# Optimization experiments

Hardware: AMD Instinct MI355X
Metric: run time of the kernel (lower is better)

The kernel has to match this reference:

```python
import jax, jax.numpy as jnp
import numpy as np
from jax import lax

INV_SQRT2 = np.float32(1.0 / np.sqrt(2.0))

def conv2d(x, w, b=None, stride=1, pad=0):
    y = lax.conv_general_dilated(x, w, (stride, stride), [(pad, pad), (pad, pad)],
                                 dimension_numbers=('NCHW', 'OIHW', 'NCHW'))
    return y if b is None else y + b[None, :, None, None]

def haar_dwt2_zero(x):
    # pytorch_wavelets DWTForward(J=1, wave='haar', mode='zero') for odd H,W:
    # pad one zero at the end of each spatial dim, then pairwise Haar analysis.
    x = jnp.pad(x, ((0, 0), (0, 0), (0, 1), (0, 1)))
    xe, xo = x[..., 0::2], x[..., 1::2]
    lo_w, hi_w = (xe + xo) * INV_SQRT2, (xe - xo) * INV_SQRT2
    def rows(t):
        te, to = t[:, :, 0::2, :], t[:, :, 1::2, :]
        return (te + to) * INV_SQRT2, (te - to) * INV_SQRT2
    ll, lh = rows(lo_w)
    hl, hh = rows(hi_w)
    return ll, lh, hl, hh  # cA, cH, cV, cD

def pixel_shuffle2(x):
    B, C, H, W = x.shape
    co = C // 4
    return x.reshape(B, co, 2, 2, H, W).transpose(0, 1, 4, 2, 5, 3).reshape(B, co, H * 2, W * 2)

def gaussian_kernel5(sigma=0.5):
    r = np.arange(5, dtype=np.float64) - 2.0
    k = np.exp(-(r ** 2) / (2.0 * sigma * sigma))
    return jnp.asarray((k / k.sum()).astype(np.float32))

_GK = gaussian_kernel5(0.5)

def gaussian_blur5(x4d):
    # cv2.GaussianBlur ksize=(5,5) sigma=0.5, default BORDER_REFLECT_101 -> 'reflect' pad
    p = jnp.pad(x4d, ((0, 0), (0, 0), (2, 2), (2, 2)), mode='reflect')
    p = conv2d(p, _GK.reshape(1, 1, 5, 1))
    return conv2d(p, _GK.reshape(1, 1, 1, 5))

def channel_attention(x, w1, w2):
    avg = jnp.mean(x, axis=(2, 3), keepdims=True)
    mx = jnp.max(x, axis=(2, 3), keepdims=True)
    mlp = lambda v: conv2d(jax.nn.relu(conv2d(v, w1)), w2)
    return jax.nn.sigmoid(mlp(avg) + mlp(mx)) * x

def _forward(x, w_x1, b_x1, w_x2, b_x2, w_x3, b_x3, w_hi, b_hi, w_lo, b_lo,
             ca1_w1, ca1_w2, ca2_w1, ca2_w2, w_cat, b_cat, w_c9a, b_c9a, w_c9b, b_c9b):
    f1 = jax.nn.relu(conv2d(x, w_x1, b_x1))            # (1,16,H,W)
    f2 = jax.nn.relu(conv2d(f1, w_x2, b_x2))           # (1,8,H,W)
    tmp12 = jax.nn.relu(conv2d(f2, w_x3, b_x3))        # (1,1,H,W)
    cA, cH, cV, cD = haar_dwt2_zero(tmp12)             # each (1,1,(H+1)/2,(W+1)/2)
    hf = pixel_shuffle2(jax.nn.relu(conv2d(jnp.concatenate([cH, cV, cD], 1), w_hi, b_hi, pad=1)))
    lf = pixel_shuffle2(jax.nn.relu(conv2d(cA, w_lo, b_lo, pad=1)))  # (1,1,H+5,W+5)
    # original detaches hf (cpu->numpy->cv2->cuda): gradients do not flow through it
    hf = gaussian_blur5(lax.stop_gradient(hf))
    hf = channel_attention(hf, ca1_w1, ca1_w2)
    lf = channel_attention(lf, ca2_w1, ca2_w2)
    alpha = 1.0
    cat = jax.nn.relu(conv2d(jnp.concatenate([alpha * hf, (1.0 - alpha) * lf], 1), w_cat, b_cat))
    f12 = tmp12 + cat                                   # (1,1,H,W)
    h = jax.nn.relu(conv2d(f12, w_c9a, b_c9a, pad=1))   # (1,32,H,W)
    return jax.nn.relu(conv2d(h, w_c9b, b_c9b, pad=1))  # (1,64,H,W)

def setup_inputs() -> dict:
    key = jax.random.key(0)
    ks = jax.random.split(key, 24)
    f32 = jnp.float32
    n = lambda k, s, sc=0.05: jax.random.normal(k, s, f32) * sc
    H = W = 511
    return {
        'x': jax.random.normal(ks[0], (1, 204, H, W), f32),
        'w_x1': n(ks[1], (16, 204, 1, 1)), 'b_x1': n(ks[2], (16,)),
        'w_x2': n(ks[3], (8, 16, 1, 1)),   'b_x2': n(ks[4], (8,)),
        'w_x3': n(ks[5], (1, 8, 1, 1)),    'b_x3': n(ks[6], (1,)),
        'w_hi': n(ks[7], (4, 3, 1, 1)),    'b_hi': n(ks[8], (4,)),
        'w_lo': n(ks[9], (4, 1, 1, 1)),    'b_lo': n(ks[10], (4,)),
        'ca1_w1': n(ks[11], (1, 1, 1, 1), 0.5), 'ca1_w2': n(ks[12], (1, 1, 1, 1), 0.5),
        'ca2_w1': n(ks[13], (1, 1, 1, 1), 0.5), 'ca2_w2': n(ks[14], (1, 1, 1, 1), 0.5),
        'w_cat': n(ks[15], (1, 2, 6, 6)),  'b_cat': n(ks[16], (1,)),
        'w_c9a': n(ks[17], (32, 1, 3, 3)), 'b_c9a': n(ks[18], (32,)),
        'w_c9b': n(ks[19], (64, 32, 3, 3)), 'b_c9b': n(ks[20], (64,)),
    }

def reference(x, w_x1, b_x1, w_x2, b_x2, w_x3, b_x3, w_hi, b_hi, w_lo, b_lo,
              ca1_w1, ca1_w2, ca2_w1, ca2_w2, w_cat, b_cat, w_c9a, b_c9a, w_c9b, b_c9b):
    return _forward(x, w_x1, b_x1, w_x2, b_x2, w_x3, b_x3, w_hi, b_hi, w_lo, b_lo,
                    ca1_w1, ca1_w2, ca2_w1, ca2_w2, w_cat, b_cat, w_c9a, b_c9a, w_c9b, b_c9b)
```

## Files before the change

kernel.cpp:

```cpp
#include <hip/hip_runtime.h>
#include <math.h>

#define NP   261121
#define HALF 130561
#define WPX  520
#define ROWN 4160
#define PSTR 2138240

typedef __attribute__((ext_vector_type(8))) short short8;
typedef __attribute__((ext_vector_type(4))) float f32x4;

static __device__ __forceinline__ unsigned short f2bf(float f) {
    unsigned int u = __builtin_bit_cast(unsigned int, f);
    u += 0x7FFFu + ((u >> 16) & 1u);
    return (unsigned short)(u >> 16);
}

__global__ __launch_bounds__(256) void k_prep(const float* __restrict__ w_c9a,
                                              const float* __restrict__ w_c9b,
                                              const float* __restrict__ w_x1,
                                              float* __restrict__ wTa,
                                              unsigned short* __restrict__ wb2,
                                              float* __restrict__ wT1,
                                              unsigned short* __restrict__ h2)
{
    int t = blockIdx.x * 256 + threadIdx.x;
    if (t < 288)  wTa[t] = w_c9a[(t & 31) * 9 + (t >> 5)];
    if (t < 3264) wT1[t] = w_x1[(t & 15) * 204 + (t >> 4)];
    if (t < 18432) {
        int o = t / 288, ck = t - o * 288;
        int c = ck / 9, k = ck - c * 9;
        wb2[k * 2048 + o * 32 + c] = f2bf(w_c9b[t]);
    }
    short8 z8 = {0, 0, 0, 0, 0, 0, 0, 0};
    if (t < 4160) {
        int pl = t / 1040;
        int rr = t - pl * 1040;
        int row = rr >= 520 ? 512 : 0;
        int ch  = rr >= 520 ? rr - 520 : rr;
        *reinterpret_cast<short8*>(h2 + (size_t)pl * PSTR + (size_t)row * ROWN + ch * 8) = z8;
    }
    int z = t - 4160;
    if (z >= 0 && z < 6132) {
        int row = z / 12 + 1;
        int j = z - (row - 1) * 12;
        int pl = j / 3, cidx = j - pl * 3;
        int col = (cidx == 0) ? 0 : (cidx == 1 ? 512 : 513);
        *reinterpret_cast<short8*>(h2 + (size_t)pl * PSTR + (size_t)row * ROWN + col * 8) = z8;
    }
}

__global__ __launch_bounds__(512) void k_conv123(const float* __restrict__ x,
                                                 const float* __restrict__ wT1,
                                                 const float* __restrict__ b1,
                                                 const float* __restrict__ w2,
                                                 const float* __restrict__ b2,
                                                 const float* __restrict__ w3,
                                                 const float* __restrict__ b3,
                                                 float* __restrict__ tmp12)
{
    __shared__ float sw[3264];
    int t = threadIdx.x;
    for (int i = t; i < 3264; i += 512) sw[i] = wT1[i];
    __syncthreads();

    int g = blockIdx.x * 512 + t;
    if (g >= HALF) return;
    int p0 = g, p1 = g + HALF;
    bool has1 = p1 < NP;
    int p1c = has1 ? p1 : p0;

    float acc0[16], acc1[16];
#pragma unroll
    for (int o = 0; o < 16; ++o) { acc0[o] = 0.f; acc1[o] = 0.f; }

#pragma unroll 4
    for (int c = 0; c < 204; ++c) {
        float xv0 = x[c * NP + p0];
        float xv1 = x[c * NP + p1c];
        const float4* wv = reinterpret_cast<const float4*>(sw + c * 16);
        float wl[16];
        *reinterpret_cast<float4*>(&wl[0])  = wv[0];
        *reinterpret_cast<float4*>(&wl[4])  = wv[1];
        *reinterpret_cast<float4*>(&wl[8])  = wv[2];
        *reinterpret_cast<float4*>(&wl[12]) = wv[3];
#pragma unroll
        for (int o = 0; o < 16; ++o) {
            acc0[o] = fmaf(xv0, wl[o], acc0[o]);
            acc1[o] = fmaf(xv1, wl[o], acc1[o]);
        }
    }

    float r0 = b3[0], r1 = b3[0];
    {
        float f10[16], f11[16];
#pragma unroll
        for (int o = 0; o < 16; ++o) {
            float bo = b1[o];
            f10[o] = fmaxf(acc0[o] + bo, 0.f);
            f11[o] = fmaxf(acc1[o] + bo, 0.f);
        }
#pragma unroll
        for (int j = 0; j < 8; ++j) {
            float s0 = b2[j], s1 = b2[j];
#pragma unroll
            for (int o = 0; o < 16; ++o) {
                float w = w2[j * 16 + o];
                s0 = fmaf(f10[o], w, s0);
                s1 = fmaf(f11[o], w, s1);
            }
            float wj = w3[j];
            r0 = fmaf(fmaxf(s0, 0.f), wj, r0);
            r1 = fmaf(fmaxf(s1, 0.f), wj, r1);
        }
    }
    tmp12[p0] = fmaxf(r0, 0.f);
    if (has1) tmp12[p1] = fmaxf(r1, 0.f);
}

__global__ __launch_bounds__(256) void k_dwt_hi(const float* __restrict__ tmp12,
                                                const float* __restrict__ w_hi,
                                                const float* __restrict__ b_hi,
                                                float* __restrict__ hf)
{
    const float INV = 0.70710678118654752440f;
    int idx = blockIdx.x * 256 + threadIdx.x;
    if (idx >= 258 * 258) return;
    int h = idx / 258, w = idx - h * 258;

    float wh[12], bh[4];
#pragma unroll
    for (int i = 0; i < 12; ++i) wh[i] = w_hi[i];
#pragma unroll
    for (int o = 0; o < 4; ++o) bh[o] = b_hi[o];

    float v[4];
    if (h == 0 || h == 257 || w == 0 || w == 257) {
#pragma unroll
        for (int o = 0; o < 4; ++o) v[o] = fmaxf(bh[o], 0.f);
    } else {
        int hh = h - 1, ww = w - 1;
        int r0 = 2 * hh, r1 = 2 * hh + 1, c0 = 2 * ww, c1 = 2 * ww + 1;
        float a = tmp12[r0 * 511 + c0];
        float b = (c1 < 511) ? tmp12[r0 * 511 + c1] : 0.f;
        float c = (r1 < 511) ? tmp12[r1 * 511 + c0] : 0.f;
        float d = (r1 < 511 && c1 < 511) ? tmp12[r1 * 511 + c1] : 0.f;
        float lo0 = (a + b) * INV, hi0 = (a - b) * INV;
        float lo1 = (c + d) * INV, hi1 = (c - d) * INV;
        float cH = (lo0 - lo1) * INV;
        float cV = (hi0 + hi1) * INV;
        float cD = (hi0 - hi1) * INV;
#pragma unroll
        for (int o = 0; o < 4; ++o)
            v[o] = fmaxf(wh[o * 3 + 0] * cH + wh[o * 3 + 1] * cV + wh[o * 3 + 2] * cD + bh[o], 0.f);
    }
    int orow = (2 * h) * 516 + 2 * w;
    hf[orow]       = v[0];
    hf[orow + 1]   = v[1];
    hf[orow + 516] = v[2];
    hf[orow + 517] = v[3];
}

__global__ __launch_bounds__(256) void k_blur(const float* __restrict__ hf,
                                              float* __restrict__ hfb,
                                              float g0, float g1, float g2)
{
    int idx = blockIdx.x * 256 + threadIdx.x;
    if (idx >= 516 * 516) return;
    int y = idx / 516, x = idx - y * 516;
    float g[5] = {g0, g1, g2, g1, g0};
    int ry[5], rx[5];
#pragma unroll
    for (int i = 0; i < 5; ++i) {
        int yy = y + i - 2; yy = yy < 0 ? -yy : (yy > 515 ? 1030 - yy : yy);
        int xx = x + i - 2; xx = xx < 0 ? -xx : (xx > 515 ? 1030 - xx : xx);
        ry[i] = yy * 516; rx[i] = xx;
    }
    float s = 0.f;
#pragma unroll
    for (int i = 0; i < 5; ++i) {
        float rs = 0.f;
#pragma unroll
        for (int j = 0; j < 5; ++j) rs = fmaf(g[j], hf[ry[i] + rx[j]], rs);
        s = fmaf(g[i], rs, s);
    }
    hfb[idx] = s;
}

__global__ __launch_bounds__(256) void k_red1(const float* __restrict__ hfb,
                                              float* __restrict__ psum,
                                              float* __restrict__ pmax)
{
    __shared__ float ss[256], sm[256];
    int t = threadIdx.x;
    int gid = blockIdx.x * 256 + t;
    float s = 0.f, m = -3.4e38f;
    for (int i = gid; i < 516 * 516; i += 65536) { float v = hfb[i]; s += v; m = fmaxf(m, v); }
    ss[t] = s; sm[t] = m;
    __syncthreads();
    for (int off = 128; off > 0; off >>= 1) {
        if (t < off) { ss[t] += ss[t + off]; sm[t] = fmaxf(sm[t], sm[t + off]); }
        __syncthreads();
    }
    if (t == 0) { psum[blockIdx.x] = ss[0]; pmax[blockIdx.x] = sm[0]; }
}

__global__ __launch_bounds__(256) void k_red2(const float* __restrict__ psum,
                                              const float* __restrict__ pmax,
                                              const float* __restrict__ caw1,
                                              const float* __restrict__ caw2,
                                              float* __restrict__ scale)
{
    __shared__ float ss[256], sm[256];
    int t = threadIdx.x;
    ss[t] = psum[t]; sm[t] = pmax[t];
    __syncthreads();
    for (int off = 128; off > 0; off >>= 1) {
        if (t < off) { ss[t] += ss[t + off]; sm[t] = fmaxf(sm[t], sm[t + off]); }
        __syncthreads();
    }
    if (t == 0) {
        float avg = ss[0] / 266256.f;
        float mx = sm[0];
        float a = caw1[0], b = caw2[0];
        float z = b * fmaxf(a * avg, 0.f) + b * fmaxf(a * mx, 0.f);
        scale[0] = 1.f / (1.f + expf(-z));
    }
}

__global__ __launch_bounds__(256) void k_cat(const float* __restrict__ hfb,
                                             const float* __restrict__ tmp12,
                                             const float* __restrict__ w_cat,
                                             const float* __restrict__ b_cat,
                                             const float* __restrict__ scale,
                                             float* __restrict__ f12)
{
    int p = blockIdx.x * 256 + threadIdx.x;
    if (p >= NP) return;
    int y = p / 511, x = p - y * 511;
    float sc = scale[0];
    float s = 0.f;
#pragma unroll
    for (int ky = 0; ky < 6; ++ky) {
        const float* row = hfb + (y + ky) * 516 + x;
#pragma unroll
        for (int kx = 0; kx < 6; ++kx) s = fmaf(row[kx], w_cat[ky * 6 + kx], s);
    }
    f12[p] = tmp12[p] + fmaxf(sc * s + b_cat[0], 0.f);
}

__global__ __launch_bounds__(256) void k_c9a(const float* __restrict__ f12,
                                             const float* __restrict__ wTa,
                                             const float* __restrict__ bias,
                                             unsigned short* __restrict__ h2)
{
    int p = blockIdx.x * 256 + threadIdx.x;
    if (p >= NP) return;
    int y = p / 511, x = p - y * 511;
    float hv[9];
#pragma unroll
    for (int ky = 0; ky < 3; ++ky)
#pragma unroll
        for (int kx = 0; kx < 3; ++kx) {
            int yy = y + ky - 1, xx = x + kx - 1;
            hv[ky * 3 + kx] = (yy >= 0 && yy < 511 && xx >= 0 && xx < 511) ? f12[yy * 511 + xx] : 0.f;
        }
    float acc[32];
#pragma unroll
    for (int o = 0; o < 32; ++o) acc[o] = bias[o];
#pragma unroll
    for (int k = 0; k < 9; ++k) {
        float v = hv[k];
        const float* wp = wTa + k * 32;
#pragma unroll
        for (int o = 0; o < 32; ++o) acc[o] = fmaf(v, wp[o], acc[o]);
    }
    unsigned short o16[32];
#pragma unroll
    for (int o = 0; o < 32; ++o) o16[o] = f2bf(fmaxf(acc[o], 0.f));
    size_t px = (size_t)(y + 1) * WPX + (x + 1);
#pragma unroll
    for (int i = 0; i < 4; ++i)
        *reinterpret_cast<short8*>(h2 + (size_t)i * PSTR + px * 8) =
            reinterpret_cast<const short8*>(o16)[i];
}

__global__ __launch_bounds__(256, 2) void k_c9b(const unsigned short* __restrict__ h2,
                                                const unsigned short* __restrict__ wb2,
                                                const float* __restrict__ bias,
                                                float* __restrict__ out)
{
    int bid = blockIdx.x;
    int xcd = bid & 7, jj = bid >> 3;
    const int q = 127, r = 6;
    int wg = (xcd < r ? xcd * (q + 1) : r * (q + 1) + (xcd - r) * q) + jj;

    int wave = threadIdx.x >> 6, lane = threadIdx.x & 63;
    int y  = wg >> 1;
    int xh = wg & 1;
    int xb = xh * 256 + wave * 64;
    int lpx = lane & 15, kg = lane >> 4;

    f32x4 acc[4][4];
#pragma unroll
    for (int m = 0; m < 4; ++m)
#pragma unroll
        for (int n = 0; n < 4; ++n) acc[m][n] = (f32x4){0.f, 0.f, 0.f, 0.f};

    const size_t pbase = (size_t)kg * PSTR;
    const int base_px = (y + 1) * WPX + (xb + 1) + lpx;

#pragma unroll
    for (int kt = 0; kt < 9; ++kt) {
        const int dy = kt / 3 - 1, dx = kt % 3 - 1;
        const int tpx = dy * WPX + dx;

        short8 a[4], b[4];
        const short8* wp = reinterpret_cast<const short8*>(wb2 + kt * 2048 + kg * 8);
#pragma unroll
        for (int m = 0; m < 4; ++m) a[m] = wp[(m * 16 + lpx) * 4];
#pragma unroll
        for (int n = 0; n < 4; ++n)
            b[n] = *reinterpret_cast<const short8*>(h2 + pbase + (size_t)(base_px + tpx + n * 16) * 8);
#pragma unroll
        for (int m = 0; m < 4; ++m)
#pragma unroll
            for (int n = 0; n < 4; ++n)
                acc[m][n] = __builtin_amdgcn_mfma_f32_16x16x32_bf16(a[m], b[n], acc[m][n], 0, 0, 0);
    }

    const int ybase = y * 511;
#pragma unroll
    for (int m = 0; m < 4; ++m) {
#pragma unroll
        for (int rr = 0; rr < 4; ++rr) {
            int o = m * 16 + kg * 4 + rr;
            float bo = bias[o];
#pragma unroll
            for (int n = 0; n < 4; ++n) {
                int px = xb + n * 16 + lpx;
                if (px < 511)
                    out[(size_t)o * NP + ybase + px] = fmaxf(acc[m][n][rr] + bo, 0.f);
            }
        }
    }
}

extern "C" void kernel_launch(void* const* d_in, const int* in_sizes, int n_in,
                              void* d_out, int out_size, void* d_ws, size_t ws_size,
                              hipStream_t stream)
{
    (void)in_sizes; (void)n_in; (void)out_size; (void)ws_size;

    const float* x     = (const float*)d_in[0];
    const float* w_x1  = (const float*)d_in[1];
    const float* b_x1  = (const float*)d_in[2];
    const float* w_x2  = (const float*)d_in[3];
    const float* b_x2  = (const float*)d_in[4];
    const float* w_x3  = (const float*)d_in[5];
    const float* b_x3  = (const float*)d_in[6];
    const float* w_hi  = (const float*)d_in[7];
    const float* b_hi  = (const float*)d_in[8];
    const float* ca1w1 = (const float*)d_in[11];
    const float* ca1w2 = (const float*)d_in[12];
    const float* w_cat = (const float*)d_in[15];
    const float* b_cat = (const float*)d_in[16];
    const float* w_c9a = (const float*)d_in[17];
    const float* b_c9a = (const float*)d_in[18];
    const float* w_c9b = (const float*)d_in[19];
    const float* b_c9b = (const float*)d_in[20];

    float* ws    = (float*)d_ws;
    float* tmp12 = ws + 0;
    float* hf    = ws + 261184;
    float* hfb   = ws + 527488;
    float* f12   = ws + 793792;
    float* psum  = ws + 1054976;
    float* pmax  = ws + 1055232;
    float* scale = ws + 1055488;
    float* wTa   = ws + 1055552;
    float* wT1   = ws + 1055872;
    unsigned short* wb2 = (unsigned short*)(ws + 1059200);
    unsigned short* h2  = (unsigned short*)(ws + 1068416);

    float* out = (float*)d_out;

    double kk[5], ssum = 0.0;
    for (int i = 0; i < 5; ++i) { double r = i - 2.0; kk[i] = exp(-r * r / 0.5); ssum += kk[i]; }
    float g0 = (float)(kk[0] / ssum), g1 = (float)(kk[1] / ssum), g2 = (float)(kk[2] / ssum);

    k_prep<<<72, 256, 0, stream>>>(w_c9a, w_c9b, w_x1, wTa, wb2, wT1, h2);
    k_conv123<<<256, 512, 0, stream>>>(x, wT1, b_x1, w_x2, b_x2, w_x3, b_x3, tmp12);
    k_dwt_hi<<<261, 256, 0, stream>>>(tmp12, w_hi, b_hi, hf);
    k_blur<<<1041, 256, 0, stream>>>(hf, hfb, g0, g1, g2);
    k_red1<<<256, 256, 0, stream>>>(hfb, psum, pmax);
    k_red2<<<1, 256, 0, stream>>>(psum, pmax, ca1w1, ca1w2, scale);
    k_cat<<<1021, 256, 0, stream>>>(hfb, tmp12, w_cat, b_cat, scale, f12);
    k_c9a<<<1021, 256, 0, stream>>>(f12, wTa, b_c9a, h2);
    k_c9b<<<1022, 256, 0, stream>>>(h2, wb2, b_c9b, out);
}
```

Measured before the change: 122.2 us.

## Fuse reductions into blur/cat kernels and stage conv weights in LDS

Moves the per-block sum/max partial reduction into the blur kernel and has every k_cat block redo the final reduction and sigmoid scale, removing the k_red1 and k_red2 launches and one re-read of the blurred map. The 3x3 conv MFMA kernel now copies its bf16 weights into shared memory in lane order, software-pipelines the halo loads across taps, and raises the launch-bounds occupancy hint to 3 waves per SIMD. The trade-off is redundant reduction of 1041 partials in every k_cat block, 36 KB of LDS per block, and a tighter register budget.

Measured after the change: 115.1 us. 5.9% less time.

```diff
diff --git a/kernel.cpp b/kernel.cpp
--- a/kernel.cpp
+++ b/kernel.cpp
@@ -1,11 +1,12 @@
 #include <hip/hip_runtime.h>
 #include <math.h>
 
-#define NP   261121
-#define HALF 130561
-#define WPX  520
-#define ROWN 4160
-#define PSTR 2138240
+#define NP    261121
+#define HALF  130561
+#define WPX   520
+#define ROWN  4160
+#define PSTR  2138240
+#define NBLUR 1041
 
 typedef __attribute__((ext_vector_type(8))) short short8;
 typedef __attribute__((ext_vector_type(4))) float f32x4;
@@ -163,11 +164,16 @@
 
 __global__ __launch_bounds__(256) void k_blur(const float* __restrict__ hf,
                                               float* __restrict__ hfb,
+                                              float* __restrict__ psum,
+                                              float* __restrict__ pmax,
                                               float g0, float g1, float g2)
 {
-    int idx = blockIdx.x * 256 + threadIdx.x;
-    if (idx >= 516 * 516) return;
-    int y = idx / 516, x = idx - y * 516;
+    __shared__ float ss[256], sm[256];
+    int t = threadIdx.x;
+    int idx = blockIdx.x * 256 + t;
+    bool ok = idx < 516 * 516;
+    int idc = ok ? idx : 0;
+    int y = idc / 516, x = idc - y * 516;
     float g[5] = {g0, g1, g2, g1, g0};
     int ry[5], rx[5];
 #pragma unroll
@@ -184,19 +190,10 @@
         for (int j = 0; j < 5; ++j) rs = fmaf(g[j], hf[ry[i] + rx[j]], rs);
         s = fmaf(g[i], rs, s);
     }
-    hfb[idx] = s;
-}
-
-__global__ __launch_bounds__(256) void k_red1(const float* __restrict__ hfb,
-                                              float* __restrict__ psum,
-                                              float* __restrict__ pmax)
-{
-    __shared__ float ss[256], sm[256];
-    int t = threadIdx.x;
-    int gid = blockIdx.x * 256 + t;
-    float s = 0.f, m = -3.4e38f;
-    for (int i = gid; i < 516 * 516; i += 65536) { float v = hfb[i]; s += v; m = fmaxf(m, v); }
-    ss[t] = s; sm[t] = m;
+    if (ok) hfb[idx] = s;
+
+    ss[t] = ok ? s : 0.f;
+    sm[t] = ok ? s : -3.4e38f;
     __syncthreads();
     for (int off = 128; off > 0; off >>= 1) {
         if (t < off) { ss[t] += ss[t + off]; sm[t] = fmaxf(sm[t], sm[t + off]); }
@@ -205,40 +202,40 @@
     if (t == 0) { psum[blockIdx.x] = ss[0]; pmax[blockIdx.x] = sm[0]; }
 }
 
-__global__ __launch_bounds__(256) void k_red2(const float* __restrict__ psum,
-                                              const float* __restrict__ pmax,
-                                              const float* __restrict__ caw1,
-                                              const float* __restrict__ caw2,
-                                              float* __restrict__ scale)
-{
-    __shared__ float ss[256], sm[256];
-    int t = threadIdx.x;
-    ss[t] = psum[t]; sm[t] = pmax[t];
-    __syncthreads();
-    for (int off = 128; off > 0; off >>= 1) {
-        if (t < off) { ss[t] += ss[t + off]; sm[t] = fmaxf(sm[t], sm[t + off]); }
-        __syncthreads();
-    }
-    if (t == 0) {
-        float avg = ss[0] / 266256.f;
-        float mx = sm[0];
-        float a = caw1[0], b = caw2[0];
-        float z = b * fmaxf(a * avg, 0.f) + b * fmaxf(a * mx, 0.f);
-        scale[0] = 1.f / (1.f + expf(-z));
-    }
-}
-
 __global__ __launch_bounds__(256) void k_cat(const float* __restrict__ hfb,
                                              const float* __restrict__ tmp12,
+                                             const float* __restrict__ psum,
+                                             const float* __restrict__ pmax,
+                                             const float* __restrict__ caw1,
+                                             const float* __restrict__ caw2,
                                              const float* __restrict__ w_cat,
                                              const float* __restrict__ b_cat,
-                                             const float* __restrict__ scale,
                                              float* __restrict__ f12)
 {
-    int p = blockIdx.x * 256 + threadIdx.x;
+    __shared__ float ss[256], sm[256], ssc;
+    int t = threadIdx.x;
+    {
+        float s = 0.f, m = -3.4e38f;
+        for (int i = t; i < NBLUR; i += 256) { s += psum[i]; m = fmaxf(m, pmax[i]); }
+        ss[t] = s; sm[t] = m;
+        __syncthreads();
+        for (int off = 128; off > 0; off >>= 1) {
+            if (t < off) { ss[t] += ss[t + off]; sm[t] = fmaxf(sm[t], sm[t + off]); }
+            __syncthreads();
+        }
+        if (t == 0) {
+            float avg = ss[0] / 266256.f;
+            float a = caw1[0], b = caw2[0];
+            float z = b * fmaxf(a * avg, 0.f) + b * fmaxf(a * sm[0], 0.f);
+            ssc = 1.f / (1.f + expf(-z));
+        }
+        __syncthreads();
+    }
+    float sc = ssc;
+
+    int p = blockIdx.x * 256 + t;
     if (p >= NP) return;
     int y = p / 511, x = p - y * 511;
-    float sc = scale[0];
     float s = 0.f;
 #pragma unroll
     for (int ky = 0; ky < 6; ++ky) {
@@ -285,49 +282,80 @@
             reinterpret_cast<const short8*>(o16)[i];
 }
 
-__global__ __launch_bounds__(256, 2) void k_c9b(const unsigned short* __restrict__ h2,
+__global__ __launch_bounds__(256, 3) void k_c9b(const unsigned short* __restrict__ h2,
                                                 const unsigned short* __restrict__ wb2,
                                                 const float* __restrict__ bias,
                                                 float* __restrict__ out)
 {
+    __shared__ unsigned short swu[9 * 2048];
+
     int bid = blockIdx.x;
     int xcd = bid & 7, jj = bid >> 3;
     const int q = 127, r = 6;
     int wg = (xcd < r ? xcd * (q + 1) : r * (q + 1) + (xcd - r) * q) + jj;
 
-    int wave = threadIdx.x >> 6, lane = threadIdx.x & 63;
+    int lane = threadIdx.x & 63;
+    int wave = threadIdx.x >> 6;
     int y  = wg >> 1;
     int xh = wg & 1;
     int xb = xh * 256 + wave * 64;
     int lpx = lane & 15, kg = lane >> 4;
 
+    {
+        const short8* wsrc = reinterpret_cast<const short8*>(wb2);
+        short8* wdst = reinterpret_cast<short8*>(swu);
+        for (int d = threadIdx.x; d < 2304; d += 256) {
+            int kt = d >> 8, rem = d & 255, m = rem >> 6, l = rem & 63;
+            wdst[d] = wsrc[kt * 256 + (m * 16 + (l & 15)) * 4 + (l >> 4)];
+        }
+    }
+    __syncthreads();
+
     f32x4 acc[4][4];
 #pragma unroll
     for (int m = 0; m < 4; ++m)
 #pragma unroll
         for (int n = 0; n < 4; ++n) acc[m][n] = (f32x4){0.f, 0.f, 0.f, 0.f};
 
-    const size_t pbase = (size_t)kg * PSTR;
+    const unsigned short* hb = h2 + (size_t)kg * PSTR;
     const int base_px = (y + 1) * WPX + (xb + 1) + lpx;
-
-#pragma unroll
-    for (int kt = 0; kt < 9; ++kt) {
-        const int dy = kt / 3 - 1, dx = kt % 3 - 1;
-        const int tpx = dy * WPX + dx;
-
-        short8 a[4], b[4];
-        const short8* wp = reinterpret_cast<const short8*>(wb2 + kt * 2048 + kg * 8);
-#pragma unroll
-        for (int m = 0; m < 4; ++m) a[m] = wp[(m * 16 + lpx) * 4];
-#pragma unroll
-        for (int n = 0; n < 4; ++n)
-            b[n] = *reinterpret_cast<const short8*>(h2 + pbase + (size_t)(base_px + tpx + n * 16) * 8);
-#pragma unroll
-        for (int m = 0; m < 4; ++m)
-#pragma unroll
-            for (int n = 0; n < 4; ++n)
-                acc[m][n] = __builtin_amdgcn_mfma_f32_16x16x32_bf16(a[m], b[n], acc[m][n], 0, 0, 0);
-    }
+    const int rowm = base_px - WPX, row0 = base_px, rowp = base_px + WPX;
+    const short8* swv = reinterpret_cast<const short8*>(swu);
+
+#define LOADB(BUF, ROW, DX) do { \
+        const unsigned short* rp = hb + (size_t)((ROW) + (DX)) * 8; \
+        BUF[0] = *reinterpret_cast<const short8*>(rp); \
+        BUF[1] = *reinterpret_cast<const short8*>(rp + 128); \
+        BUF[2] = *reinterpret_cast<const short8*>(rp + 256); \
+        BUF[3] = *reinterpret_cast<const short8*>(rp + 384); \
+    } while (0)
+
+#define TAP(KT, BUF) do { \
+        const short8* ap = swv + (KT) * 256 + lane; \
+        short8 a0 = ap[0], a1 = ap[64], a2 = ap[128], a3 = ap[192]; \
+        _Pragma("unroll") \
+        for (int n = 0; n < 4; ++n) { \
+            acc[0][n] = __builtin_amdgcn_mfma_f32_16x16x32_bf16(a0, BUF[n], acc[0][n], 0, 0, 0); \
+            acc[1][n] = __builtin_amdgcn_mfma_f32_16x16x32_bf16(a1, BUF[n], acc[1][n], 0, 0, 0); \
+            acc[2][n] = __builtin_amdgcn_mfma_f32_16x16x32_bf16(a2, BUF[n], acc[2][n], 0, 0, 0); \
+            acc[3][n] = __builtin_amdgcn_mfma_f32_16x16x32_bf16(a3, BUF[n], acc[3][n], 0, 0, 0); \
+        } \
+    } while (0)
+
+    short8 bX[4], bY[4], bZ[4];
+    LOADB(bX, rowm, -1);
+    LOADB(bY, rowm,  0);
+    LOADB(bZ, rowm, +1); TAP(0, bX);
+    LOADB(bX, row0, -1); TAP(1, bY);
+    LOADB(bY, row0,  0); TAP(2, bZ);
+    LOADB(bZ, row0, +1); TAP(3, bX);
+    LOADB(bX, rowp, -1); TAP(4, bY);
+    LOADB(bY, rowp,  0); TAP(5, bZ);
+    LOADB(bZ, rowp, +1); TAP(6, bX);
+    TAP(7, bY);
+    TAP(8, bZ);
+#undef LOADB
+#undef TAP
 
     const int ybase = y * 511;
 #pragma unroll
@@ -376,12 +404,11 @@
     float* hfb   = ws + 527488;
     float* f12   = ws + 793792;
     float* psum  = ws + 1054976;
-    float* pmax  = ws + 1055232;
-    float* scale = ws + 1055488;
-    float* wTa   = ws + 1055552;
-    float* wT1   = ws + 1055872;
-    unsigned short* wb2 = (unsigned short*)(ws + 1059200);
-    unsigned short* h2  = (unsigned short*)(ws + 1068416);
+    float* pmax  = ws + 1056032;
+    float* wTa   = ws + 1057088;
+    float* wT1   = ws + 1057408;
+    unsigned short* wb2 = (unsigned short*)(ws + 1060736);
+    unsigned short* h2  = (unsigned short*)(ws + 1069952);
 
     float* out = (float*)d_out;
 
@@ -392,10 +419,8 @@
     k_prep<<<72, 256, 0, stream>>>(w_c9a, w_c9b, w_x1, wTa, wb2, wT1, h2);
     k_conv123<<<256, 512, 0, stream>>>(x, wT1, b_x1, w_x2, b_x2, w_x3, b_x3, tmp12);
     k_dwt_hi<<<261, 256, 0, stream>>>(tmp12, w_hi, b_hi, hf);
-    k_blur<<<1041, 256, 0, stream>>>(hf, hfb, g0, g1, g2);
-    k_red1<<<256, 256, 0, stream>>>(hfb, psum, pmax);
-    k_red2<<<1, 256, 0, stream>>>(psum, pmax, ca1w1, ca1w2, scale);
-    k_cat<<<1021, 256, 0, stream>>>(hfb, tmp12, w_cat, b_cat, scale, f12);
+    k_blur<<<NBLUR, 256, 0, stream>>>(hf, hfb, psum, pmax, g0, g1, g2);
+    k_cat<<<1021, 256, 0, stream>>>(hfb, tmp12, psum, pmax, ca1w1, ca1w2, w_cat, b_cat, f12);
     k_c9a<<<1021, 256, 0, stream>>>(f12, wTa, b_c9a, h2);
     k_c9b<<<1022, 256, 0, stream>>>(h2, wb2, b_c9b, out);
 }
```
